# Performance work log

Measured on AMD Instinct MI355X. Metric: run time of the kernel, lower is better.

Reference implementation:

```python
import jax, jax.numpy as jnp
import numpy as np

LREL = 0.01  # LeakyReLU default negative_slope

L, D, B = 256, 64, 32


def setup_inputs() -> dict:
    key = jax.random.key(0)
    ks = jax.random.split(key, 10)
    return {
        "emb": jax.random.normal(ks[0], (B, L * D + 1), jnp.float32),
        "tw": jax.random.normal(ks[1], (L * D + 1,), jnp.float32) * 0.02,
        "tb": jax.random.normal(ks[2], (1,), jnp.float32) * 0.02,
        "w1": jax.random.normal(ks[3], (D, 2 * D), jnp.float32) * (1.0 / np.sqrt(2 * D)),
        "b1": jax.random.normal(ks[4], (D,), jnp.float32) * 0.02,
        "w2": jax.random.normal(ks[5], (16, D), jnp.float32) * (1.0 / np.sqrt(D)),
        "b2": jax.random.normal(ks[6], (16,), jnp.float32) * 0.02,
        "w3": jax.random.normal(ks[7], (1, 16), jnp.float32) * 0.25,
        "b3": jax.random.normal(ks[8], (1,), jnp.float32) * 0.02,
        "scale": jnp.array([0.2], jnp.float32),
    }


def reference(emb, tw, tb, w1, b1, w2, b2, w3, b3, scale):
    # first-order term: Linear(L*D+1 -> 1), squeezed
    x1 = emb @ tw + tb[0]  # [B]

    x2 = emb[:, :-1].reshape(emb.shape[0], L, D)  # [B,L,D]
    mask = (jnp.abs(x2).sum(-1) > 0).astype(emb.dtype)  # [B,L]
    pmask = mask[:, :, None] * mask[:, None, :]  # [B,L,L]

    w = tw[:-1].reshape(1, L, D)
    x2 = x2 * w

    xi = x2[:, :, None, :]  # [B,L,1,D]
    xj = x2[:, None, :, :]  # [B,1,L,D]
    feat = jnp.concatenate(
        [jnp.broadcast_to((xi + xj) * 0.5, (emb.shape[0], L, L, D)),
         jnp.broadcast_to(jnp.abs(xi - xj), (emb.shape[0], L, L, D))],
        axis=-1)  # [B,L,L,2D]

    h = jax.nn.leaky_relu(jnp.einsum('bijf,df->bijd', feat, w1) + b1, LREL)
    h = jax.nn.leaky_relu(jnp.einsum('bijd,kd->bijk', h, w2) + b2, LREL)
    s = (jnp.einsum('bijk,ok->bijo', h, w3) + b3)[..., 0]  # [B,L,L]

    s = s * pmask
    s = jnp.triu(s, k=1).sum(axis=(1, 2)) * scale[0]  # [B]
    return x1 + s
```

## Files before the change

kernel.cpp:

```cpp
#include <hip/hip_runtime.h>

typedef _Float16 half8  __attribute__((ext_vector_type(8)));
typedef _Float16 half2v __attribute__((ext_vector_type(2)));
typedef short    s16x8  __attribute__((ext_vector_type(8)));
typedef float    f32x4  __attribute__((ext_vector_type(4)));

#define LL 256
#define DD 64
#define BB 32
#define LREL 0.01f
#define EMBC (LL*DD + 1)
#define NTILE 72
#define NBLK_MAIN (BB * NTILE)

__global__ void k_prep_all(const float* __restrict__ emb, const float* __restrict__ tw,
                           const float* __restrict__ w1, const float* __restrict__ w2,
                           _Float16* __restrict__ y16, float* __restrict__ maskw,
                           _Float16* __restrict__ w1h, _Float16* __restrict__ w2h,
                           float* __restrict__ x1part, float* __restrict__ bc)
{
    int blk = blockIdx.x, tid = threadIdx.x;
    if (blk < 2048) {
        int lin = blk * 4 + (tid >> 6);
        int lane = tid & 63;
        int b = lin >> 8, l = lin & 255;
        float e = emb[(size_t)b * EMBC + l * 64 + lane];
        float t = tw[l * 64 + lane];
        y16[((size_t)(b * 256 + l)) * 64 + lane] = (_Float16)(e * t * 0.5f);
        float a = fabsf(e);
        #pragma unroll
        for (int m = 32; m; m >>= 1) a += __shfl_xor(a, m, 64);
        if (lane == 0) maskw[b * 256 + l] = (a > 0.f) ? 1.f : 0.f;
    } else if (blk < 2084) {
        int idx = (blk - 2048) * 256 + tid;
        if (idx < 8192) {
            float v = w1[idx];
            if ((idx & 127) >= 64) v *= 2.f;
            w1h[idx] = (_Float16)v;
        } else if (idx < 9216) {
            w2h[idx - 8192] = (_Float16)w2[idx - 8192];
        }
        if (blk == 2048 && tid < 33) bc[tid] = 0.f;
    } else {
        int bl = blk - 2084;
        int b = bl >> 2, q = bl & 3;
        const float* row = emb + (size_t)b * EMBC;
        int cend = (q + 1) * 4097; if (cend > EMBC) cend = EMBC;
        float part = 0.f;
        for (int c = q * 4097 + tid; c < cend; c += 256) part = fmaf(row[c], tw[c], part);
        __shared__ float red[256];
        red[tid] = part; __syncthreads();
        for (int s = 128; s; s >>= 1) { if (tid < s) red[tid] += red[tid + s]; __syncthreads(); }
        if (tid == 0) x1part[bl] = red[0];
    }
}

__global__ __launch_bounds__(128) void k_main(
    const _Float16* __restrict__ y16, const float* __restrict__ maskw,
    const _Float16* __restrict__ w1h, const _Float16* __restrict__ w2h,
    const float* __restrict__ b1, const float* __restrict__ b2,
    const float* __restrict__ w3, const float* __restrict__ b3,
    const float* __restrict__ x1part, const float* __restrict__ tb,
    const float* __restrict__ scale, float* __restrict__ bc,
    float* __restrict__ out)
{
    const int tid = threadIdx.x;
    const int lane = tid & 63, wid = tid >> 6;
    const int g = lane >> 4, p = lane & 15;

    const int blk = blockIdx.x;
    const int batch = blk / NTILE;
    const int t = blk - batch * NTILE;
    int bj, bi;
    if (t < 12)      { if (t < 2) { bj = 0; bi = t; } else if (t < 6) { bj = 1; bi = t - 2; } else { bj = 2; bi = t - 6; } }
    else if (t < 30) { if (t < 20) { bj = 3; bi = t - 12; } else { bj = 4; bi = t - 20; } }
    else             { if (t < 42) { bj = 5; bi = t - 30; } else if (t < 56) { bj = 6; bi = t - 42; } else { bj = 7; bi = t - 56; } }
    const int i0 = bi * 16, j0 = bj * 32;

    __shared__ _Float16 yi_s[16][72];
    __shared__ _Float16 yj_s[32][72];
    __shared__ _Float16 h1_s[2][16][72];
    __shared__ float mi_s[16], mj_s[32];
    __shared__ int lastflag;

    const _Float16* ybase = y16 + (size_t)batch * (LL * DD);
    for (int r = tid; r < 48 * 8; r += 128) {
        int row = r >> 3, c = r & 7;
        int pos = (row < 16) ? (i0 + row) : (j0 + row - 16);
        float4 v = *(const float4*)(ybase + pos * 64 + c * 8);
        if (row < 16) *(float4*)&yi_s[row][c * 8] = v;
        else          *(float4*)&yj_s[row - 16][c * 8] = v;
    }
    if (tid < 16)      mi_s[tid]      = maskw[batch * LL + i0 + tid];
    else if (tid < 48) mj_s[tid - 16] = maskw[batch * LL + j0 + tid - 16];
    __syncthreads();

    half8 w1f[4][4];
    #pragma unroll
    for (int T = 0; T < 4; ++T)
        #pragma unroll
        for (int kb = 0; kb < 4; ++kb)
            w1f[T][kb] = *(const half8*)(w1h + (T * 16 + p) * 128 + kb * 32 + g * 8);
    half8 w2f[2];
    #pragma unroll
    for (int kb = 0; kb < 2; ++kb)
        w2f[kb] = *(const half8*)(w2h + p * 64 + kb * 32 + g * 8);

    f32x4 b1v[4];
    #pragma unroll
    for (int T = 0; T < 4; ++T) b1v[T] = *(const f32x4*)(b1 + T * 16 + g * 4);
    const f32x4 b2v = *(const f32x4*)(b2 + g * 4);
    const f32x4 w3v = *(const f32x4*)(w3 + g * 4);
    const float b3v = (g == 0) ? b3[0] : 0.f;

    const int jl = wid * 16 + p;
    const int jglob = j0 + jl;
    const float mj = mj_s[jl];
    const half8 yjA = *(const half8*)&yj_s[jl][g * 8];
    const half8 yjB = *(const half8*)&yj_s[jl][32 + g * 8];

    const int jmax = j0 + wid * 16 + 15;
    int nil = jmax - i0; if (nil > 16) nil = 16;

    const half2v lrel2 = {(_Float16)LREL, (_Float16)LREL};
    const half2v zero2 = {};

    float sacc = 0.f;
    for (int il = 0; il < nil; ++il) {
        const int i = i0 + il;
        const half8 yiA = *(const half8*)&yi_s[il][g * 8];
        const half8 yiB = *(const half8*)&yi_s[il][32 + g * 8];

        half8 f0 = yiA + yjA;
        half8 f1 = yiB + yjB;
        s16x8 ad0 = __builtin_bit_cast(s16x8, yiA - yjA) & (short)0x7FFF;
        s16x8 ad1 = __builtin_bit_cast(s16x8, yiB - yjB) & (short)0x7FFF;
        half8 f2 = __builtin_bit_cast(half8, ad0);
        half8 f3 = __builtin_bit_cast(half8, ad1);

        f32x4 acc[4] = {b1v[0], b1v[1], b1v[2], b1v[3]};
        #pragma unroll
        for (int T = 0; T < 4; ++T) {
            acc[T] = __builtin_amdgcn_mfma_f32_16x16x32_f16(w1f[T][0], f0, acc[T], 0, 0, 0);
            acc[T] = __builtin_amdgcn_mfma_f32_16x16x32_f16(w1f[T][1], f1, acc[T], 0, 0, 0);
            acc[T] = __builtin_amdgcn_mfma_f32_16x16x32_f16(w1f[T][2], f2, acc[T], 0, 0, 0);
            acc[T] = __builtin_amdgcn_mfma_f32_16x16x32_f16(w1f[T][3], f3, acc[T], 0, 0, 0);
        }

        #pragma unroll
        for (int T = 0; T < 4; ++T) {
            half2v a = __builtin_bit_cast(half2v, __builtin_amdgcn_cvt_pkrtz(acc[T][0], acc[T][1]));
            half2v b = __builtin_bit_cast(half2v, __builtin_amdgcn_cvt_pkrtz(acc[T][2], acc[T][3]));
            a = __builtin_elementwise_max(a, zero2) + lrel2 * __builtin_elementwise_min(a, zero2);
            b = __builtin_elementwise_max(b, zero2) + lrel2 * __builtin_elementwise_min(b, zero2);
            *(unsigned*)&h1_s[wid][p][T * 16 + g * 4]     = __builtin_bit_cast(unsigned, a);
            *(unsigned*)&h1_s[wid][p][T * 16 + g * 4 + 2] = __builtin_bit_cast(unsigned, b);
        }

        const half8 hB0 = *(const half8*)&h1_s[wid][p][g * 8];
        const half8 hB1 = *(const half8*)&h1_s[wid][p][32 + g * 8];

        f32x4 a2 = b2v;
        a2 = __builtin_amdgcn_mfma_f32_16x16x32_f16(w2f[0], hB0, a2, 0, 0, 0);
        a2 = __builtin_amdgcn_mfma_f32_16x16x32_f16(w2f[1], hB1, a2, 0, 0, 0);

        float sp = b3v;
        #pragma unroll
        for (int r = 0; r < 4; ++r) {
            float h = a2[r];
            h = fmaxf(h, 0.f) + LREL * fminf(h, 0.f);
            sp = fmaf(h, w3v[r], sp);
        }
        const float mfac = (jglob > i) ? (mi_s[il] * mj) : 0.f;
        sacc = fmaf(sp, mfac, sacc);
    }

    #pragma unroll
    for (int m = 32; m; m >>= 1) sacc += __shfl_xor(sacc, m, 64);
    if (lane == 0) atomicAdd(&bc[batch], sacc);

    __syncthreads();
    if (tid == 0) {
        __threadfence();
        float old = atomicAdd(&bc[32], 1.0f);
        lastflag = (old >= (float)(NBLK_MAIN - 1)) ? 1 : 0;
    }
    __syncthreads();
    if (lastflag && tid < BB) {
        float bs = atomicAdd(&bc[tid], 0.0f);
        float x1 = x1part[tid * 4] + x1part[tid * 4 + 1] + x1part[tid * 4 + 2]
                 + x1part[tid * 4 + 3] + tb[0];
        out[tid] = fmaf(bs, scale[0], x1);
    }
}

extern "C" void kernel_launch(void* const* d_in, const int* in_sizes, int n_in,
                              void* d_out, int out_size, void* d_ws, size_t ws_size,
                              hipStream_t stream)
{
    const float* emb   = (const float*)d_in[0];
    const float* tw    = (const float*)d_in[1];
    const float* tb    = (const float*)d_in[2];
    const float* w1    = (const float*)d_in[3];
    const float* b1    = (const float*)d_in[4];
    const float* w2    = (const float*)d_in[5];
    const float* b2    = (const float*)d_in[6];
    const float* w3    = (const float*)d_in[7];
    const float* b3    = (const float*)d_in[8];
    const float* scale = (const float*)d_in[9];

    char* ws = (char*)d_ws;
    _Float16* y16   = (_Float16*)(ws + 0);
    float*    maskw = (float*)(ws + 1048576);
    _Float16* w1h   = (_Float16*)(ws + 1081344);
    _Float16* w2h   = (_Float16*)(ws + 1097728);
    float*    x1part= (float*)(ws + 1099776);
    float*    bc    = (float*)(ws + 1100288);
    float*    out   = (float*)d_out;

    hipLaunchKernelGGL(k_prep_all, dim3(2048 + 36 + 128), dim3(256), 0, stream,
                       emb, tw, w1, w2, y16, maskw, w1h, w2h, x1part, bc);
    hipLaunchKernelGGL(k_main, dim3(NBLK_MAIN), dim3(128), 0, stream,
                       y16, maskw, w1h, w2h, b1, b2, w3, b3, x1part, tb, scale, bc, out);
}
```

Before: 154.1 us.

## Fuse preprocessing into main kernel and replace atomics with per-block partials

Removes the separate prep kernel. The main kernel now loads fp32 emb and tw directly, computes the row masks and the scaled fp16 tiles itself, and converts w1 and w2 to fp16 fragments in registers. The layer-1 output is repacked in registers as the B operand for the second MFMA, so it no longer goes through shared memory. Global atomics and the last-block detection are replaced by per-block partial sums, which a small finalize kernel reduces together with the first-order dot product. The cost is redundant per-block weight conversion and emb reads, and mask sums computed serially by 48 threads. The scale by 0.5 also moves from y to the w1 weights, and the register repack assumes a particular MFMA output/input lane layout.

```diff
diff --git a/kernel.cpp b/kernel.cpp
--- a/kernel.cpp
+++ b/kernel.cpp
@@ -4,6 +4,7 @@
 typedef _Float16 half2v __attribute__((ext_vector_type(2)));
 typedef short    s16x8  __attribute__((ext_vector_type(8)));
 typedef float    f32x4  __attribute__((ext_vector_type(4)));
+typedef int      i32x4  __attribute__((ext_vector_type(4)));
 
 #define LL 256
 #define DD 64
@@ -13,56 +14,12 @@
 #define NTILE 72
 #define NBLK_MAIN (BB * NTILE)
 
-__global__ void k_prep_all(const float* __restrict__ emb, const float* __restrict__ tw,
-                           const float* __restrict__ w1, const float* __restrict__ w2,
-                           _Float16* __restrict__ y16, float* __restrict__ maskw,
-                           _Float16* __restrict__ w1h, _Float16* __restrict__ w2h,
-                           float* __restrict__ x1part, float* __restrict__ bc)
-{
-    int blk = blockIdx.x, tid = threadIdx.x;
-    if (blk < 2048) {
-        int lin = blk * 4 + (tid >> 6);
-        int lane = tid & 63;
-        int b = lin >> 8, l = lin & 255;
-        float e = emb[(size_t)b * EMBC + l * 64 + lane];
-        float t = tw[l * 64 + lane];
-        y16[((size_t)(b * 256 + l)) * 64 + lane] = (_Float16)(e * t * 0.5f);
-        float a = fabsf(e);
-        #pragma unroll
-        for (int m = 32; m; m >>= 1) a += __shfl_xor(a, m, 64);
-        if (lane == 0) maskw[b * 256 + l] = (a > 0.f) ? 1.f : 0.f;
-    } else if (blk < 2084) {
-        int idx = (blk - 2048) * 256 + tid;
-        if (idx < 8192) {
-            float v = w1[idx];
-            if ((idx & 127) >= 64) v *= 2.f;
-            w1h[idx] = (_Float16)v;
-        } else if (idx < 9216) {
-            w2h[idx - 8192] = (_Float16)w2[idx - 8192];
-        }
-        if (blk == 2048 && tid < 33) bc[tid] = 0.f;
-    } else {
-        int bl = blk - 2084;
-        int b = bl >> 2, q = bl & 3;
-        const float* row = emb + (size_t)b * EMBC;
-        int cend = (q + 1) * 4097; if (cend > EMBC) cend = EMBC;
-        float part = 0.f;
-        for (int c = q * 4097 + tid; c < cend; c += 256) part = fmaf(row[c], tw[c], part);
-        __shared__ float red[256];
-        red[tid] = part; __syncthreads();
-        for (int s = 128; s; s >>= 1) { if (tid < s) red[tid] += red[tid + s]; __syncthreads(); }
-        if (tid == 0) x1part[bl] = red[0];
-    }
-}
-
 __global__ __launch_bounds__(128) void k_main(
-    const _Float16* __restrict__ y16, const float* __restrict__ maskw,
-    const _Float16* __restrict__ w1h, const _Float16* __restrict__ w2h,
-    const float* __restrict__ b1, const float* __restrict__ b2,
+    const float* __restrict__ emb, const float* __restrict__ tw,
+    const float* __restrict__ w1, const float* __restrict__ b1,
+    const float* __restrict__ w2, const float* __restrict__ b2,
     const float* __restrict__ w3, const float* __restrict__ b3,
-    const float* __restrict__ x1part, const float* __restrict__ tb,
-    const float* __restrict__ scale, float* __restrict__ bc,
-    float* __restrict__ out)
+    float* __restrict__ part)
 {
     const int tid = threadIdx.x;
     const int lane = tid & 63, wid = tid >> 6;
@@ -77,34 +34,62 @@
     else             { if (t < 42) { bj = 5; bi = t - 30; } else if (t < 56) { bj = 6; bi = t - 42; } else { bj = 7; bi = t - 56; } }
     const int i0 = bi * 16, j0 = bj * 32;
 
-    __shared__ _Float16 yi_s[16][72];
-    __shared__ _Float16 yj_s[32][72];
-    __shared__ _Float16 h1_s[2][16][72];
-    __shared__ float mi_s[16], mj_s[32];
-    __shared__ int lastflag;
-
-    const _Float16* ybase = y16 + (size_t)batch * (LL * DD);
-    for (int r = tid; r < 48 * 8; r += 128) {
-        int row = r >> 3, c = r & 7;
+    __shared__ _Float16 yts[48][72];
+    __shared__ float masks[48];
+    __shared__ float wsum[2];
+
+    const float* erow = emb + (size_t)batch * EMBC;
+
+    if (tid < 48) {
+        int pos = (tid < 16) ? (i0 + tid) : (j0 + tid - 16);
+        const float* r = erow + pos * 64;
+        float a = 0.f;
+        #pragma unroll 8
+        for (int c = 0; c < 64; ++c) a += fabsf(r[c]);
+        masks[tid] = (a > 0.f) ? 1.f : 0.f;
+    }
+
+    for (int k = 0; k < 24; ++k) {
+        int idx = k * 128 + tid;
+        int row = idx >> 6, col = idx & 63;
         int pos = (row < 16) ? (i0 + row) : (j0 + row - 16);
-        float4 v = *(const float4*)(ybase + pos * 64 + c * 8);
-        if (row < 16) *(float4*)&yi_s[row][c * 8] = v;
-        else          *(float4*)&yj_s[row - 16][c * 8] = v;
-    }
-    if (tid < 16)      mi_s[tid]      = maskw[batch * LL + i0 + tid];
-    else if (tid < 48) mj_s[tid - 16] = maskw[batch * LL + j0 + tid - 16];
-    __syncthreads();
+        float e = erow[pos * 64 + col];
+        float tt = tw[pos * 64 + col];
+        yts[row][col] = (_Float16)(e * tt);
+    }
 
     half8 w1f[4][4];
     #pragma unroll
-    for (int T = 0; T < 4; ++T)
-        #pragma unroll
-        for (int kb = 0; kb < 4; ++kb)
-            w1f[T][kb] = *(const half8*)(w1h + (T * 16 + p) * 128 + kb * 32 + g * 8);
+    for (int T = 0; T < 4; ++T) {
+        #pragma unroll
+        for (int kb = 0; kb < 4; ++kb) {
+            const float* src = w1 + (T * 16 + p) * 128 + kb * 32 + g * 8;
+            f32x4 lo = *(const f32x4*)src;
+            f32x4 hi = *(const f32x4*)(src + 4);
+            const float s = (kb < 2) ? 0.5f : 1.0f;
+            half8 h;
+            #pragma unroll
+            for (int e = 0; e < 4; ++e) {
+                h[e]     = (_Float16)(lo[e] * s);
+                h[e + 4] = (_Float16)(hi[e] * s);
+            }
+            w1f[T][kb] = h;
+        }
+    }
     half8 w2f[2];
     #pragma unroll
-    for (int kb = 0; kb < 2; ++kb)
-        w2f[kb] = *(const half8*)(w2h + p * 64 + kb * 32 + g * 8);
+    for (int kb = 0; kb < 2; ++kb) {
+        const float* r2 = w2 + p * 64;
+        f32x4 lo = *(const f32x4*)(r2 + (2 * kb) * 16 + g * 4);
+        f32x4 hi = *(const f32x4*)(r2 + (2 * kb + 1) * 16 + g * 4);
+        half8 h;
+        #pragma unroll
+        for (int e = 0; e < 4; ++e) {
+            h[e]     = (_Float16)lo[e];
+            h[e + 4] = (_Float16)hi[e];
+        }
+        w2f[kb] = h;
+    }
 
     f32x4 b1v[4];
     #pragma unroll
@@ -113,14 +98,16 @@
     const f32x4 w3v = *(const f32x4*)(w3 + g * 4);
     const float b3v = (g == 0) ? b3[0] : 0.f;
 
+    __syncthreads();
+
     const int jl = wid * 16 + p;
     const int jglob = j0 + jl;
-    const float mj = mj_s[jl];
-    const half8 yjA = *(const half8*)&yj_s[jl][g * 8];
-    const half8 yjB = *(const half8*)&yj_s[jl][32 + g * 8];
-
-    const int jmax = j0 + wid * 16 + 15;
-    int nil = jmax - i0; if (nil > 16) nil = 16;
+    const float mj = masks[16 + jl];
+    const half8 yjA = *(const half8*)&yts[16 + jl][g * 8];
+    const half8 yjB = *(const half8*)&yts[16 + jl][32 + g * 8];
+
+    const int jmaxv = j0 + wid * 16 + 15;
+    int nil = jmaxv - i0; if (nil > 16) nil = 16;
 
     const half2v lrel2 = {(_Float16)LREL, (_Float16)LREL};
     const half2v zero2 = {};
@@ -128,8 +115,8 @@
     float sacc = 0.f;
     for (int il = 0; il < nil; ++il) {
         const int i = i0 + il;
-        const half8 yiA = *(const half8*)&yi_s[il][g * 8];
-        const half8 yiB = *(const half8*)&yi_s[il][32 + g * 8];
+        const half8 yiA = *(const half8*)&yts[il][g * 8];
+        const half8 yiB = *(const half8*)&yts[il][32 + g * 8];
 
         half8 f0 = yiA + yjA;
         half8 f1 = yiB + yjB;
@@ -147,18 +134,21 @@
             acc[T] = __builtin_amdgcn_mfma_f32_16x16x32_f16(w1f[T][3], f3, acc[T], 0, 0, 0);
         }
 
+        unsigned hv[4][2];
         #pragma unroll
         for (int T = 0; T < 4; ++T) {
             half2v a = __builtin_bit_cast(half2v, __builtin_amdgcn_cvt_pkrtz(acc[T][0], acc[T][1]));
             half2v b = __builtin_bit_cast(half2v, __builtin_amdgcn_cvt_pkrtz(acc[T][2], acc[T][3]));
             a = __builtin_elementwise_max(a, zero2) + lrel2 * __builtin_elementwise_min(a, zero2);
             b = __builtin_elementwise_max(b, zero2) + lrel2 * __builtin_elementwise_min(b, zero2);
-            *(unsigned*)&h1_s[wid][p][T * 16 + g * 4]     = __builtin_bit_cast(unsigned, a);
-            *(unsigned*)&h1_s[wid][p][T * 16 + g * 4 + 2] = __builtin_bit_cast(unsigned, b);
-        }
-
-        const half8 hB0 = *(const half8*)&h1_s[wid][p][g * 8];
-        const half8 hB1 = *(const half8*)&h1_s[wid][p][32 + g * 8];
+            hv[T][0] = __builtin_bit_cast(unsigned, a);
+            hv[T][1] = __builtin_bit_cast(unsigned, b);
+        }
+
+        i32x4 R0 = {(int)hv[0][0], (int)hv[0][1], (int)hv[1][0], (int)hv[1][1]};
+        i32x4 R1 = {(int)hv[2][0], (int)hv[2][1], (int)hv[3][0], (int)hv[3][1]};
+        half8 hB0 = __builtin_bit_cast(half8, R0);
+        half8 hB1 = __builtin_bit_cast(half8, R1);
 
         f32x4 a2 = b2v;
         a2 = __builtin_amdgcn_mfma_f32_16x16x32_f16(w2f[0], hB0, a2, 0, 0, 0);
@@ -171,27 +161,30 @@
             h = fmaxf(h, 0.f) + LREL * fminf(h, 0.f);
             sp = fmaf(h, w3v[r], sp);
         }
-        const float mfac = (jglob > i) ? (mi_s[il] * mj) : 0.f;
+        const float mfac = (jglob > i) ? (masks[il] * mj) : 0.f;
         sacc = fmaf(sp, mfac, sacc);
     }
 
     #pragma unroll
     for (int m = 32; m; m >>= 1) sacc += __shfl_xor(sacc, m, 64);
-    if (lane == 0) atomicAdd(&bc[batch], sacc);
-
+    if (lane == 0) wsum[wid] = sacc;
     __syncthreads();
-    if (tid == 0) {
-        __threadfence();
-        float old = atomicAdd(&bc[32], 1.0f);
-        lastflag = (old >= (float)(NBLK_MAIN - 1)) ? 1 : 0;
-    }
-    __syncthreads();
-    if (lastflag && tid < BB) {
-        float bs = atomicAdd(&bc[tid], 0.0f);
-        float x1 = x1part[tid * 4] + x1part[tid * 4 + 1] + x1part[tid * 4 + 2]
-                 + x1part[tid * 4 + 3] + tb[0];
-        out[tid] = fmaf(bs, scale[0], x1);
-    }
+    if (tid == 0) part[blk] = wsum[0] + wsum[1];
+}
+
+__global__ void k_fin(const float* __restrict__ emb, const float* __restrict__ tw,
+                      const float* __restrict__ tb, const float* __restrict__ scale,
+                      const float* __restrict__ part, float* __restrict__ out)
+{
+    const int b = blockIdx.x, tid = threadIdx.x;
+    const float* row = emb + (size_t)b * EMBC;
+    float s = 0.f;
+    for (int c = tid; c < EMBC; c += 256) s = fmaf(row[c], tw[c], s);
+    if (tid < NTILE) s += scale[0] * part[b * NTILE + tid];
+    __shared__ float red[256];
+    red[tid] = s; __syncthreads();
+    for (int st = 128; st; st >>= 1) { if (tid < st) red[tid] += red[tid + st]; __syncthreads(); }
+    if (tid == 0) out[b] = red[0] + tb[0];
 }
 
 extern "C" void kernel_launch(void* const* d_in, const int* in_sizes, int n_in,
@@ -209,17 +202,11 @@
     const float* b3    = (const float*)d_in[8];
     const float* scale = (const float*)d_in[9];
 
-    char* ws = (char*)d_ws;
-    _Float16* y16   = (_Float16*)(ws + 0);
-    float*    maskw = (float*)(ws + 1048576);
-    _Float16* w1h   = (_Float16*)(ws + 1081344);
-    _Float16* w2h   = (_Float16*)(ws + 1097728);
-    float*    x1part= (float*)(ws + 1099776);
-    float*    bc    = (float*)(ws + 1100288);
-    float*    out   = (float*)d_out;
-
-    hipLaunchKernelGGL(k_prep_all, dim3(2048 + 36 + 128), dim3(256), 0, stream,
-                       emb, tw, w1, w2, y16, maskw, w1h, w2h, x1part, bc);
+    float* part = (float*)d_ws;
+    float* out  = (float*)d_out;
+
     hipLaunchKernelGGL(k_main, dim3(NBLK_MAIN), dim3(128), 0, stream,
-                       y16, maskw, w1h, w2h, b1, b2, w3, b3, x1part, tb, scale, bc, out);
+                       emb, tw, w1, b1, w2, b2, w3, b3, part);
+    hipLaunchKernelGGL(k_fin, dim3(BB), dim3(256), 0, stream,
+                       emb, tw, tb, scale, part, out);
 }
```

Result: faster. 144.4 us (-6.3%).
